# Kernel tuning notes

Hardware: AMD Instinct MI355X
Metric: run time of the kernel (lower is better)

Reference implementation:

```python
import jax, jax.numpy as jnp
import numpy as np

N_HEAD = 16
N_KV_HEAD = 4
HEAD_DIM = 128
EPS = 1e-6


def apply_rotary_emb(x, cos, sin):
    # x: (B,T,H,hd); cos/sin: (1,T,1,hd//2)
    d = x.shape[3] // 2
    x1, x2 = x[..., :d], x[..., d:]
    y1 = x1 * cos + x2 * sin
    y2 = x1 * -sin + x2 * cos
    return jnp.concatenate([y1, y2], axis=3).astype(x.dtype)


def rmsnorm(x):
    # flax nnx.RMSNorm with use_scale=False: x * rsqrt(mean(x^2) + eps)
    ms = jnp.mean(jnp.square(x), axis=-1, keepdims=True)
    return (x * jax.lax.rsqrt(ms + EPS)).astype(x.dtype)


def setup_inputs() -> dict:
    key = jax.random.key(0)
    ks = jax.random.split(key, 7)
    B, T, C = 4, 2048, 2048
    s = 0.02
    return {
        "x": jax.random.normal(ks[0], (B, T, C), jnp.float32),
        "cos": jax.random.normal(ks[1], (1, T, 1, HEAD_DIM // 2), jnp.float32),
        "sin": jax.random.normal(ks[2], (1, T, 1, HEAD_DIM // 2), jnp.float32),
        "Wq": jax.random.normal(ks[3], (C, N_HEAD * HEAD_DIM), jnp.float32) * s,
        "Wk": jax.random.normal(ks[4], (C, N_KV_HEAD * HEAD_DIM), jnp.float32) * s,
        "Wv": jax.random.normal(ks[5], (C, N_KV_HEAD * HEAD_DIM), jnp.float32) * s,
        "Wo": jax.random.normal(ks[6], (C, C), jnp.float32) * s,
    }


def reference(x, cos, sin, Wq, Wk, Wv, Wo):
    B, T, C = x.shape
    q = (x @ Wq).reshape(B, T, N_HEAD, HEAD_DIM)
    k = (x @ Wk).reshape(B, T, N_KV_HEAD, HEAD_DIM)
    v = (x @ Wv).reshape(B, T, N_KV_HEAD, HEAD_DIM)
    q = rmsnorm(apply_rotary_emb(q, cos, sin))
    k = rmsnorm(apply_rotary_emb(k, cos, sin))
    # (B,H,T,hd)
    q = jnp.transpose(q, (0, 2, 1, 3))
    k = jnp.transpose(k, (0, 2, 1, 3))
    v = jnp.transpose(v, (0, 2, 1, 3))
    nrep = N_HEAD // N_KV_HEAD
    k = jnp.repeat(k, nrep, axis=1)
    v = jnp.repeat(v, nrep, axis=1)
    scale = 1.0 / jnp.sqrt(jnp.float32(HEAD_DIM))
    att = jnp.einsum('bhqd,bhkd->bhqk', q, k) * scale
    mask = jnp.tril(jnp.ones((T, T), dtype=bool))[None, None, :, :]
    att = jnp.where(mask, att, -jnp.inf)
    att = jax.nn.softmax(att, axis=-1)
    y = jnp.einsum('bhqk,bhkd->bhqd', att, v)
    y = jnp.transpose(y, (0, 2, 1, 3)).reshape(B, T, -1)
    return y @ Wo
```

## Files before the change

### kernel.cpp

```cpp
#include <hip/hip_runtime.h>
#include <hip/hip_bf16.h>

typedef __attribute__((ext_vector_type(8))) short short8;
typedef __attribute__((ext_vector_type(4))) float f32x4;

#define B_SZ 4
#define T_SEQ 2048
#define C_DIM 2048
#define NH 16
#define NKV 4
#define HD 128

#define MFMA16 __builtin_amdgcn_mfma_f32_16x16x32_bf16

__device__ __forceinline__ unsigned short f2bf(float f) {
  union { __hip_bfloat16 h; unsigned short u; } v;
  v.h = __float2bfloat16(f);
  return v.u;
}
__device__ __forceinline__ float bf2f(unsigned short u) {
  union { unsigned short u; __hip_bfloat16 h; } v;
  v.u = u;
  return __bfloat162float(v.h);
}

__device__ __forceinline__ void gload_lds16(const unsigned short* g, unsigned short* l) {
  __builtin_amdgcn_global_load_lds(
      (const __attribute__((address_space(1))) unsigned int*)g,
      (__attribute__((address_space(3))) unsigned int*)l, 16, 0, 0);
}

__global__ void cast_x(const float* __restrict__ x, unsigned short* __restrict__ xb, int n4) {
  int i = blockIdx.x * blockDim.x + threadIdx.x;
  if (i < n4) {
    float4 f = ((const float4*)x)[i];
    ushort4 u = make_ushort4(f2bf(f.x), f2bf(f.y), f2bf(f.z), f2bf(f.w));
    ((ushort4*)xb)[i] = u;
  }
}

__global__ void wtrans(const float* __restrict__ W, unsigned short* __restrict__ Wt, int K, int N) {
  __shared__ float tile[32][33];
  int k0 = blockIdx.x * 32, n0 = blockIdx.y * 32;
  int tx = threadIdx.x, ty = threadIdx.y;
#pragma unroll
  for (int i = 0; i < 4; i++)
    tile[ty + i * 8][tx] = W[(size_t)(k0 + ty + i * 8) * N + n0 + tx];
  __syncthreads();
#pragma unroll
  for (int i = 0; i < 4; i++)
    Wt[(size_t)(n0 + ty + i * 8) * K + k0 + tx] = f2bf(tile[tx][ty + i * 8]);
}

__global__ void vtrans(const unsigned short* __restrict__ qkv, unsigned short* __restrict__ Vt) {
  __shared__ unsigned short tile[32][34];
  int t0 = blockIdx.x * 32, d0 = blockIdx.y * 32;
  int b = blockIdx.z >> 2, kvh = blockIdx.z & 3;
  int tx = threadIdx.x, ty = threadIdx.y;
#pragma unroll
  for (int i = 0; i < 4; i++)
    tile[ty + i * 8][tx] =
        qkv[(size_t)(b * T_SEQ + t0 + ty + i * 8) * 3072 + 2560 + kvh * HD + d0 + tx];
  __syncthreads();
#pragma unroll
  for (int i = 0; i < 4; i++)
    Vt[((size_t)(b * NKV + kvh) * HD + d0 + ty + i * 8) * T_SEQ + t0 + tx] = tile[tx][ty + i * 8];
}

template <typename OutT>
__global__ __launch_bounds__(512, 2) void gemm256(const unsigned short* __restrict__ A,
                                                  const unsigned short* __restrict__ Bt,
                                                  OutT* __restrict__ Cc, int N, int K, int GX) {
  __shared__ alignas(16) unsigned short lds[2][4][128 * 64];
  const int tid = threadIdx.x, lane = tid & 63, wid = tid >> 6;
  const int wave_m = wid >> 2, wave_n = wid & 3;
  const int r16 = lane & 15, q4 = lane >> 4;
  const int sw = r16 & 7;

  int nwg = gridDim.x, orig = blockIdx.x;
  int qq = nwg >> 3, rr = nwg & 7;
  int xcd = orig & 7, loc = orig >> 3;
  int wg = (xcd < rr ? xcd * (qq + 1) : rr * (qq + 1) + (xcd - rr) * qq) + loc;
  int bx = wg % GX, by = wg / GX;
  const size_t row0 = (size_t)bx * 256, col0 = (size_t)by * 256;

  const unsigned short* Ab0 = A + row0 * K;
  const unsigned short* Ab1 = A + (row0 + 128) * K;
  const unsigned short* Bb0 = Bt + col0 * K;
  const unsigned short* Bb1 = Bt + (col0 + 128) * K;

  const int srow = lane >> 3, spb = lane & 7;
  auto stage = [&](const unsigned short* base, int buf, int slot, int k0) {
#pragma unroll
    for (int j = 0; j < 2; ++j) {
      int cw = j * 8 + wid;
      int row = cw * 8 + srow;
      gload_lds16(base + (size_t)row * K + k0 + ((spb ^ srow) * 8), &lds[buf][slot][cw * 512]);
    }
  };

  f32x4 acc[8][4];
  f32x4 zero = {0.f, 0.f, 0.f, 0.f};
#pragma unroll
  for (int m = 0; m < 8; m++)
#pragma unroll
    for (int n = 0; n < 4; n++) acc[m][n] = zero;

  const int NT = K / 64;
  stage(Ab0, 0, 0, 0);
  stage(Ab1, 0, 1, 0);
  stage(Bb0, 0, 2, 0);
  stage(Bb1, 0, 3, 0);
  stage(Ab0, 1, 0, 64);
  stage(Ab1, 1, 1, 64);
  asm volatile("s_waitcnt vmcnt(4)" ::: "memory");
  __builtin_amdgcn_s_barrier();

  short8 af[4][2], b01[2][2], b23[2][2];
  const int bslot = 2 + (wave_n >> 1);
  const int bro = (wave_n & 1) * 64;

  int cur = 0;
#pragma unroll 1
  for (int t = 0; t < NT; ++t) {
    const unsigned short* Ah = &lds[cur][wave_m][0];
    const unsigned short* Bh = &lds[cur][bslot][0];
    const int k1 = t * 64 + 64, k2 = t * 64 + 128;
#pragma unroll
    for (int mf = 0; mf < 4; mf++)
#pragma unroll
      for (int kk = 0; kk < 2; kk++)
        af[mf][kk] = *(const short8*)(Ah + (mf * 16 + r16) * 64 + (((kk * 4 + q4) ^ sw) * 8));
#pragma unroll
    for (int nf = 0; nf < 2; nf++)
#pragma unroll
      for (int kk = 0; kk < 2; kk++)
        b01[nf][kk] =
            *(const short8*)(Bh + (bro + nf * 16 + r16) * 64 + (((kk * 4 + q4) ^ sw) * 8));
    if (t + 1 < NT) stage(Bb0, cur ^ 1, 2, k1);
    __builtin_amdgcn_s_barrier();
    asm volatile("s_waitcnt lgkmcnt(0)" ::: "memory");
    __builtin_amdgcn_s_setprio(1);
#pragma unroll
    for (int mf = 0; mf < 4; mf++)
#pragma unroll
      for (int nf = 0; nf < 2; nf++)
#pragma unroll
        for (int kk = 0; kk < 2; kk++)
          acc[mf][nf] = MFMA16(af[mf][kk], b01[nf][kk], acc[mf][nf], 0, 0, 0);
    __builtin_amdgcn_s_setprio(0);
    __builtin_amdgcn_s_barrier();
#pragma unroll
    for (int nf = 0; nf < 2; nf++)
#pragma unroll
      for (int kk = 0; kk < 2; kk++)
        b23[nf][kk] =
            *(const short8*)(Bh + (bro + (nf + 2) * 16 + r16) * 64 + (((kk * 4 + q4) ^ sw) * 8));
    if (t + 1 < NT) stage(Bb1, cur ^ 1, 3, k1);
    __builtin_amdgcn_s_barrier();
    asm volatile("s_waitcnt lgkmcnt(0)" ::: "memory");
    __builtin_amdgcn_s_setprio(1);
#pragma unroll
    for (int mf = 0; mf < 4; mf++)
#pragma unroll
      for (int nf = 0; nf < 2; nf++)
#pragma unroll
        for (int kk = 0; kk < 2; kk++)
          acc[mf][nf + 2] = MFMA16(af[mf][kk], b23[nf][kk], acc[mf][nf + 2], 0, 0, 0);
    __builtin_amdgcn_s_setprio(0);
    __builtin_amdgcn_s_barrier();
#pragma unroll
    for (int mf = 0; mf < 4; mf++)
#pragma unroll
      for (int kk = 0; kk < 2; kk++)
        af[mf][kk] =
            *(const short8*)(Ah + ((mf + 4) * 16 + r16) * 64 + (((kk * 4 + q4) ^ sw) * 8));
    __builtin_amdgcn_s_barrier();
    asm volatile("s_waitcnt lgkmcnt(0)" ::: "memory");
    __builtin_amdgcn_s_setprio(1);
#pragma unroll
    for (int mf = 0; mf < 4; mf++)
#pragma unroll
      for (int nf = 0; nf < 2; nf++)
#pragma unroll
        for (int kk = 0; kk < 2; kk++)
          acc[mf + 4][nf] = MFMA16(af[mf][kk], b01[nf][kk], acc[mf + 4][nf], 0, 0, 0);
    __builtin_amdgcn_s_setprio(0);
    __builtin_amdgcn_s_barrier();
    if (t + 2 < NT) {
      stage(Ab0, cur, 0, k2);
      stage(Ab1, cur, 1, k2);
    }
    __builtin_amdgcn_s_barrier();
    __builtin_amdgcn_s_setprio(1);
#pragma unroll
    for (int mf = 0; mf < 4; mf++)
#pragma unroll
      for (int nf = 0; nf < 2; nf++)
#pragma unroll
        for (int kk = 0; kk < 2; kk++)
          acc[mf + 4][nf + 2] = MFMA16(af[mf][kk], b23[nf][kk], acc[mf + 4][nf + 2], 0, 0, 0);
    __builtin_amdgcn_s_setprio(0);
    if (t + 1 < NT) {
      if (t + 2 < NT)
        asm volatile("s_waitcnt vmcnt(4)" ::: "memory");
      else
        asm volatile("s_waitcnt vmcnt(0)" ::: "memory");
    }
    __builtin_amdgcn_s_barrier();
    cur ^= 1;
  }

#pragma unroll
  for (int mf = 0; mf < 8; mf++)
#pragma unroll
    for (int nf = 0; nf < 4; nf++) {
      size_t rbase = row0 + wave_m * 128 + mf * 16 + q4 * 4;
      size_t cc = col0 + wave_n * 64 + nf * 16 + r16;
#pragma unroll
      for (int jj = 0; jj < 4; jj++) {
        if constexpr (sizeof(OutT) == 2)
          Cc[(rbase + jj) * (size_t)N + cc] = f2bf(acc[mf][nf][jj]);
        else
          Cc[(rbase + jj) * (size_t)N + cc] = acc[mf][nf][jj];
      }
    }
}

template <int NHEADS>
__global__ void ropenorm(const unsigned short* __restrict__ qkv, int colbase,
                         const float* __restrict__ cosp, const float* __restrict__ sinp,
                         unsigned short* __restrict__ qout, float outscale) {
  int gid = blockIdx.x * 4 + (threadIdx.x >> 6);
  int lane = threadIdx.x & 63;
  int h = gid % NHEADS;
  int bt = gid / NHEADS;
  int t = bt % T_SEQ, b = bt / T_SEQ;
  const unsigned short* src = qkv + (size_t)(b * T_SEQ + t) * 3072 + colbase + h * HD;
  float x1 = bf2f(src[lane]), x2 = bf2f(src[64 + lane]);
  float c = cosp[t * 64 + lane], s = sinp[t * 64 + lane];
  float y1 = x1 * c + x2 * s;
  float y2 = x2 * c - x1 * s;
  float ss = y1 * y1 + y2 * y2;
#pragma unroll
  for (int d = 1; d < 64; d <<= 1) ss += __shfl_xor(ss, d);
  float r = rsqrtf(ss * (1.f / 128.f) + 1e-6f) * outscale;
  unsigned short* dst = qout + ((size_t)(b * NHEADS + h) * T_SEQ + t) * HD;
  dst[lane] = f2bf(y1 * r);
  dst[64 + lane] = f2bf(y2 * r);
}

__device__ __forceinline__ int swzP(int row) {
  return (row & 7) ^ (((row >> 3) & 1) << 1);
}

__global__ __launch_bounds__(256, 2) void attn(const unsigned short* __restrict__ Qn,
                                               const unsigned short* __restrict__ Kn,
                                               const unsigned short* __restrict__ Vt,
                                               unsigned short* __restrict__ Y) {
  __shared__ alignas(16) unsigned short lK[2][64 * 128];
  __shared__ alignas(16) unsigned short lV[2][128 * 64];
  __shared__ alignas(16) unsigned short pl[4][32 * 64];

  int lin = blockIdx.x;
  int low3 = lin & 7, rest = lin >> 3;
  int chi = rest >> 6, idx = rest & 63;
  int c = (chi << 3) | low3;
  int b = c >> 2, kvh = c & 3;
  int h = kvh * 4 + (idx >> 4);
  int qt = 15 - (idx & 15);
  int Q0 = qt * 128;

  int lane = threadIdx.x & 63, w = threadIdx.x >> 6;
  const int r16 = lane & 15, q4 = lane >> 4;
  const unsigned short* Qp = Qn + ((size_t)(b * NH + h) * T_SEQ + Q0 + w * 32) * HD;
  const unsigned short* Kp = Kn + (size_t)(b * NKV + kvh) * T_SEQ * HD;
  const unsigned short* Vp = Vt + (size_t)(b * NKV + kvh) * HD * T_SEQ;

  short8 qf[2][4];
#pragma unroll
  for (int m = 0; m < 2; m++)
#pragma unroll
    for (int i = 0; i < 4; i++)
      qf[m][i] = *(const short8*)(Qp + (m * 16 + r16) * HD + i * 32 + q4 * 8);

  f32x4 zero = {0.f, 0.f, 0.f, 0.f};
  f32x4 o[2][8];
  float mrow[2][4], Lp[2][4];
#pragma unroll
  for (int m = 0; m < 2; m++) {
#pragma unroll
    for (int nb = 0; nb < 8; nb++) o[m][nb] = zero;
#pragma unroll
    for (int j = 0; j < 4; j++) { mrow[m][j] = -1e30f; Lp[m][j] = 0.f; }
  }

  auto stageK = [&](int kv0, int buf) {
#pragma unroll
    for (int j = 0; j < 4; ++j) {
      int cw = w * 4 + j;
      int row = cw * 4 + (lane >> 4);
      int cb = lane & 15;
      gload_lds16(Kp + (size_t)(kv0 + row) * HD + ((cb ^ (row & 7)) * 8), &lK[buf][cw * 512]);
    }
  };
  auto stageV = [&](int kv0, int buf) {
#pragma unroll
    for (int j = 0; j < 4; ++j) {
      int cw = w * 4 + j;
      int row = cw * 8 + (lane >> 3);
      int db = lane & 7;
      gload_lds16(Vp + (size_t)row * T_SEQ + kv0 + ((db ^ (row & 7)) * 8), &lV[buf][cw * 512]);
    }
  };

  const int ntiles = 2 * qt + 2;
  const int ntw = (Q0 + w * 32 + 95) >> 6;

  stageK(0, 0);
  stageV(0, 0);
  __syncthreads();
  int cur = 0;

  for (int t = 0; t < ntiles; ++t) {
    int kv0 = t * 64;
    if (t + 1 < ntiles) { stageK(kv0 + 64, cur ^ 1); stageV(kv0 + 64, cur ^ 1); }
    if (t < ntw) {
      f32x4 s[2][4];
      __builtin_amdgcn_s_setprio(1);
#pragma unroll
      for (int nt = 0; nt < 4; nt++) {
        f32x4 a0 = zero, a1 = zero;
        int krow = nt * 16 + r16;
#pragma unroll
        for (int i = 0; i < 4; i++) {
          short8 kf =
              *(const short8*)(&lK[cur][krow * 128 + ((q4 * 8 + i * 32) ^ ((krow & 7) << 3))]);
          a0 = __builtin_amdgcn_mfma_f32_16x16x32_bf16(qf[0][i], kf, a0, 0, 0, 0);
          a1 = __builtin_amdgcn_mfma_f32_16x16x32_bf16(qf[1][i], kf, a1, 0, 0, 0);
        }
        s[0][nt] = a0;
        s[1][nt] = a1;
      }
      __builtin_amdgcn_s_setprio(0);
      if (kv0 + 63 > Q0 + w * 32) {
#pragma unroll
        for (int m = 0; m < 2; m++)
#pragma unroll
          for (int nt = 0; nt < 4; nt++)
#pragma unroll
            for (int j = 0; j < 4; j++) {
              int col = kv0 + nt * 16 + r16;
              int row = Q0 + w * 32 + m * 16 + q4 * 4 + j;
              if (col > row) s[m][nt][j] = -1e30f;
            }
      }
      float pm[2][4];
#pragma unroll
      for (int m = 0; m < 2; m++)
#pragma unroll
        for (int j = 0; j < 4; j++)
          pm[m][j] = fmaxf(fmaxf(s[m][0][j], s[m][1][j]), fmaxf(s[m][2][j], s[m][3][j]));
#pragma unroll
      for (int d = 1; d < 16; d <<= 1)
#pragma unroll
        for (int m = 0; m < 2; m++)
#pragma unroll
          for (int j = 0; j < 4; j++) pm[m][j] = fmaxf(pm[m][j], __shfl_xor(pm[m][j], d));
      float dmax = -1e30f;
#pragma unroll
      for (int m = 0; m < 2; m++)
#pragma unroll
        for (int j = 0; j < 4; j++) dmax = fmaxf(dmax, pm[m][j] - mrow[m][j]);
      if (!__all(dmax <= 8.0f)) {
#pragma unroll
        for (int m = 0; m < 2; m++)
#pragma unroll
          for (int j = 0; j < 4; j++) {
            float mn = fmaxf(mrow[m][j], pm[m][j]);
            float al = __expf(mrow[m][j] - mn);
            mrow[m][j] = mn;
            Lp[m][j] *= al;
#pragma unroll
            for (int nb = 0; nb < 8; nb++) o[m][nb][j] *= al;
          }
      }
#pragma unroll
      for (int m = 0; m < 2; m++)
#pragma unroll
        for (int nt = 0; nt < 4; nt++)
#pragma unroll
          for (int j = 0; j < 4; j++) {
            float p = __expf(s[m][nt][j] - mrow[m][j]);
            Lp[m][j] += p;
            int prow = m * 16 + q4 * 4 + j;
            pl[w][prow * 64 + ((nt * 16 + r16) ^ (swzP(prow) << 3))] = f2bf(p);
          }
      __builtin_amdgcn_s_setprio(1);
#pragma unroll
      for (int ks = 0; ks < 2; ks++) {
        int t0 = ks * 32 + q4 * 8;
        int prow0 = r16, prow1 = 16 + r16;
        short8 pf0 = *(const short8*)(&pl[w][prow0 * 64 + (t0 ^ (swzP(prow0) << 3))]);
        short8 pf1 = *(const short8*)(&pl[w][prow1 * 64 + (t0 ^ (swzP(prow1) << 3))]);
#pragma unroll
        for (int nb = 0; nb < 8; nb++) {
          int vrow = nb * 16 + r16;
          short8 vf = *(const short8*)(&lV[cur][vrow * 64 + (t0 ^ ((vrow & 7) << 3))]);
          o[0][nb] = __builtin_amdgcn_mfma_f32_16x16x32_bf16(pf0, vf, o[0][nb], 0, 0, 0);
          o[1][nb] = __builtin_amdgcn_mfma_f32_16x16x32_bf16(pf1, vf, o[1][nb], 0, 0, 0);
        }
      }
      __builtin_amdgcn_s_setprio(0);
    }
    __syncthreads();
    cur ^= 1;
  }

  float linv[2][4];
#pragma unroll
  for (int m = 0; m < 2; m++)
#pragma unroll
    for (int j = 0; j < 4; j++) {
      float v = Lp[m][j];
#pragma unroll
      for (int d = 1; d < 16; d <<= 1) v += __shfl_xor(v, d);
      linv[m][j] = 1.f / v;
    }
#pragma unroll
  for (int m = 0; m < 2; m++)
#pragma unroll
    for (int nb = 0; nb < 8; nb++)
#pragma unroll
      for (int j = 0; j < 4; j++) {
        size_t row = (size_t)Q0 + w * 32 + m * 16 + q4 * 4 + j;
        Y[((size_t)(b * T_SEQ) + row) * (NH * HD) + h * HD + nb * 16 + r16] =
            f2bf(o[m][nb][j] * linv[m][j]);
      }
}

extern "C" void kernel_launch(void* const* d_in, const int* in_sizes, int n_in,
                              void* d_out, int out_size, void* d_ws, size_t ws_size,
                              hipStream_t stream) {
  const float* x = (const float*)d_in[0];
  const float* cosp = (const float*)d_in[1];
  const float* sinp = (const float*)d_in[2];
  const float* Wq = (const float*)d_in[3];
  const float* Wk = (const float*)d_in[4];
  const float* Wv = (const float*)d_in[5];
  const float* Wo = (const float*)d_in[6];
  float* out = (float*)d_out;

  char* ws = (char*)d_ws;
  size_t off = 0;
  auto alloc = [&](size_t bytes) { void* p = ws + off; off += bytes; return p; };
  const size_t BT = (size_t)B_SZ * T_SEQ;
  unsigned short* xb = (unsigned short*)alloc(BT * C_DIM * 2);
  unsigned short* WqkvT = (unsigned short*)alloc((size_t)3072 * 2048 * 2);
  unsigned short* WoT = (unsigned short*)alloc((size_t)2048 * 2048 * 2);
  unsigned short* qkv = (unsigned short*)alloc(BT * 3072 * 2);
  unsigned short* Kb = (unsigned short*)alloc(BT * 512 * 2);
  unsigned short* Vb = (unsigned short*)alloc(BT * 512 * 2);
  unsigned short* Qb = xb;
  unsigned short* Yb = qkv;

  dim3 tb(32, 8);
  cast_x<<<16384, 256, 0, stream>>>(x, xb, (int)(BT * C_DIM / 4));
  wtrans<<<dim3(64, 64), tb, 0, stream>>>(Wq, WqkvT, 2048, 2048);
  wtrans<<<dim3(64, 16), tb, 0, stream>>>(Wk, WqkvT + (size_t)2048 * 2048, 2048, 512);
  wtrans<<<dim3(64, 16), tb, 0, stream>>>(Wv, WqkvT + (size_t)2560 * 2048, 2048, 512);
  wtrans<<<dim3(64, 64), tb, 0, stream>>>(Wo, WoT, 2048, 2048);

  gemm256<unsigned short><<<384, 512, 0, stream>>>(xb, WqkvT, qkv, 3072, 2048, 32);

  ropenorm<NH><<<(B_SZ * T_SEQ * NH) / 4, 256, 0, stream>>>(qkv, 0, cosp, sinp, Qb,
                                                            0.08838834764831845f);
  ropenorm<NKV><<<(B_SZ * T_SEQ * NKV) / 4, 256, 0, stream>>>(qkv, 2048, cosp, sinp, Kb, 1.0f);
  vtrans<<<dim3(64, 4, 16), tb, 0, stream>>>(qkv, Vb);

  attn<<<dim3(1024), 256, 0, stream>>>(Qb, Kb, Vb, Yb);

  gemm256<float><<<256, 512, 0, stream>>>(Yb, WoT, out, 2048, 2048, 32);
}
```

Before: 434.6 us.

## Merge weight transposes and rope kernels; use 128x256 tiles for QKV GEMM

Folds the four weight-transpose launches into one kernel and the two rope/norm launches into one, which removes launch overhead and tail gaps between them. Replaces the 256x256-tile QKV projection GEMM with a new 128x256-tile kernel. That kernel splits B staging into two halves that are interleaved with MFMA phases, and it doubles the grid to 768 workgroups to fill the 256 CUs better. The cost is lower per-tile arithmetic intensity, so A and B are fetched more times per output.

```diff
diff --git a/kernel.cpp b/kernel.cpp
--- a/kernel.cpp
+++ b/kernel.cpp
@@ -39,9 +39,19 @@
   }
 }
 
-__global__ void wtrans(const float* __restrict__ W, unsigned short* __restrict__ Wt, int K, int N) {
+__global__ void wtransAll(const float* __restrict__ Wq, const float* __restrict__ Wk,
+                          const float* __restrict__ Wv, const float* __restrict__ Wo,
+                          unsigned short* __restrict__ WqkvT, unsigned short* __restrict__ WoT) {
   __shared__ float tile[32][33];
-  int k0 = blockIdx.x * 32, n0 = blockIdx.y * 32;
+  int y = blockIdx.y;
+  const float* W;
+  unsigned short* Wt;
+  int N, n0;
+  if (y < 64) { W = Wq; Wt = WqkvT; N = 2048; n0 = y * 32; }
+  else if (y < 80) { W = Wk; Wt = WqkvT + (size_t)2048 * 2048; N = 512; n0 = (y - 64) * 32; }
+  else if (y < 96) { W = Wv; Wt = WqkvT + (size_t)2560 * 2048; N = 512; n0 = (y - 80) * 32; }
+  else { W = Wo; Wt = WoT; N = 2048; n0 = (y - 96) * 32; }
+  int k0 = blockIdx.x * 32;
   int tx = threadIdx.x, ty = threadIdx.y;
 #pragma unroll
   for (int i = 0; i < 4; i++)
@@ -49,7 +59,7 @@
   __syncthreads();
 #pragma unroll
   for (int i = 0; i < 4; i++)
-    Wt[(size_t)(n0 + ty + i * 8) * K + k0 + tx] = f2bf(tile[tx][ty + i * 8]);
+    Wt[(size_t)(n0 + ty + i * 8) * 2048 + k0 + tx] = f2bf(tile[tx][ty + i * 8]);
 }
 
 __global__ void vtrans(const unsigned short* __restrict__ qkv, unsigned short* __restrict__ Vt) {
@@ -65,6 +75,130 @@
 #pragma unroll
   for (int i = 0; i < 4; i++)
     Vt[((size_t)(b * NKV + kvh) * HD + d0 + ty + i * 8) * T_SEQ + t0 + tx] = tile[tx][ty + i * 8];
+}
+
+template <typename OutT>
+__global__ __launch_bounds__(512, 2) void gemm128(const unsigned short* __restrict__ A,
+                                                  const unsigned short* __restrict__ Bt,
+                                                  OutT* __restrict__ Cc, int N, int K, int GX) {
+  __shared__ alignas(16) unsigned short lds[2][3][128 * 64];
+  const int tid = threadIdx.x, lane = tid & 63, wid = tid >> 6;
+  const int wave_m = wid >> 2, wave_n = wid & 3;
+  const int r16 = lane & 15, q4 = lane >> 4;
+  const int sw = r16 & 7;
+
+  int nwg = gridDim.x, orig = blockIdx.x;
+  int qq = nwg >> 3, rr = nwg & 7;
+  int xcd = orig & 7, loc = orig >> 3;
+  int wg = (xcd < rr ? xcd * (qq + 1) : rr * (qq + 1) + (xcd - rr) * qq) + loc;
+  int bx = wg % GX, by = wg / GX;
+  const size_t row0 = (size_t)bx * 128, col0 = (size_t)by * 256;
+
+  const unsigned short* Ab = A + row0 * K;
+  const unsigned short* Bb0 = Bt + col0 * K;
+  const unsigned short* Bb1 = Bt + (col0 + 128) * K;
+
+  const int srow = lane >> 3, spb = lane & 7;
+  auto stage = [&](const unsigned short* base, int buf, int slot, int k0) {
+#pragma unroll
+    for (int j = 0; j < 2; ++j) {
+      int cw = j * 8 + wid;
+      int row = cw * 8 + srow;
+      gload_lds16(base + (size_t)row * K + k0 + ((spb ^ srow) * 8), &lds[buf][slot][cw * 512]);
+    }
+  };
+
+  f32x4 acc[4][4];
+  f32x4 zero = {0.f, 0.f, 0.f, 0.f};
+#pragma unroll
+  for (int m = 0; m < 4; m++)
+#pragma unroll
+    for (int n = 0; n < 4; n++) acc[m][n] = zero;
+
+  const int NT = K / 64;
+  stage(Ab, 0, 0, 0);
+  stage(Bb0, 0, 1, 0);
+  stage(Bb1, 0, 2, 0);
+  stage(Ab, 1, 0, 64);
+  asm volatile("s_waitcnt vmcnt(2)" ::: "memory");
+  __builtin_amdgcn_s_barrier();
+
+  short8 af[4][2], b01[2][2], b23[2][2];
+  const int bslot = 1 + (wave_n >> 1);
+  const int bro = (wave_n & 1) * 64;
+
+  int cur = 0;
+#pragma unroll 1
+  for (int t = 0; t < NT; ++t) {
+    const unsigned short* Ah = &lds[cur][0][0];
+    const unsigned short* Bh = &lds[cur][bslot][0];
+    const int k1 = t * 64 + 64, k2 = t * 64 + 128;
+#pragma unroll
+    for (int mf = 0; mf < 4; mf++)
+#pragma unroll
+      for (int kk = 0; kk < 2; kk++)
+        af[mf][kk] =
+            *(const short8*)(Ah + (wave_m * 64 + mf * 16 + r16) * 64 + (((kk * 4 + q4) ^ sw) * 8));
+#pragma unroll
+    for (int nf = 0; nf < 2; nf++)
+#pragma unroll
+      for (int kk = 0; kk < 2; kk++)
+        b01[nf][kk] =
+            *(const short8*)(Bh + (bro + nf * 16 + r16) * 64 + (((kk * 4 + q4) ^ sw) * 8));
+    if (t + 1 < NT) stage(Bb0, cur ^ 1, 1, k1);
+    __builtin_amdgcn_s_barrier();
+    asm volatile("s_waitcnt lgkmcnt(0)" ::: "memory");
+    __builtin_amdgcn_s_setprio(1);
+#pragma unroll
+    for (int mf = 0; mf < 4; mf++)
+#pragma unroll
+      for (int nf = 0; nf < 2; nf++)
+#pragma unroll
+        for (int kk = 0; kk < 2; kk++)
+          acc[mf][nf] = MFMA16(af[mf][kk], b01[nf][kk], acc[mf][nf], 0, 0, 0);
+    __builtin_amdgcn_s_setprio(0);
+    __builtin_amdgcn_s_barrier();
+#pragma unroll
+    for (int nf = 0; nf < 2; nf++)
+#pragma unroll
+      for (int kk = 0; kk < 2; kk++)
+        b23[nf][kk] =
+            *(const short8*)(Bh + (bro + (nf + 2) * 16 + r16) * 64 + (((kk * 4 + q4) ^ sw) * 8));
+    if (t + 1 < NT) stage(Bb1, cur ^ 1, 2, k1);
+    if (t + 2 < NT) stage(Ab, cur, 0, k2);
+    __builtin_amdgcn_s_barrier();
+    asm volatile("s_waitcnt lgkmcnt(0)" ::: "memory");
+    __builtin_amdgcn_s_setprio(1);
+#pragma unroll
+    for (int mf = 0; mf < 4; mf++)
+#pragma unroll
+      for (int nf = 0; nf < 2; nf++)
+#pragma unroll
+        for (int kk = 0; kk < 2; kk++)
+          acc[mf][nf + 2] = MFMA16(af[mf][kk], b23[nf][kk], acc[mf][nf + 2], 0, 0, 0);
+    __builtin_amdgcn_s_setprio(0);
+    if (t + 2 < NT)
+      asm volatile("s_waitcnt vmcnt(2)" ::: "memory");
+    else if (t + 1 < NT)
+      asm volatile("s_waitcnt vmcnt(0)" ::: "memory");
+    __builtin_amdgcn_s_barrier();
+    cur ^= 1;
+  }
+
+#pragma unroll
+  for (int mf = 0; mf < 4; mf++)
+#pragma unroll
+    for (int nf = 0; nf < 4; nf++) {
+      size_t rbase = row0 + wave_m * 64 + mf * 16 + q4 * 4;
+      size_t cc = col0 + wave_n * 64 + nf * 16 + r16;
+#pragma unroll
+      for (int jj = 0; jj < 4; jj++) {
+        if constexpr (sizeof(OutT) == 2)
+          Cc[(rbase + jj) * (size_t)N + cc] = f2bf(acc[mf][nf][jj]);
+        else
+          Cc[(rbase + jj) * (size_t)N + cc] = acc[mf][nf][jj];
+      }
+    }
 }
 
 template <typename OutT>
@@ -227,16 +361,28 @@
     }
 }
 
-template <int NHEADS>
-__global__ void ropenorm(const unsigned short* __restrict__ qkv, int colbase,
-                         const float* __restrict__ cosp, const float* __restrict__ sinp,
-                         unsigned short* __restrict__ qout, float outscale) {
+__global__ void ropeAll(const unsigned short* __restrict__ qkv, const float* __restrict__ cosp,
+                        const float* __restrict__ sinp, unsigned short* __restrict__ Qb,
+                        unsigned short* __restrict__ Kb) {
   int gid = blockIdx.x * 4 + (threadIdx.x >> 6);
   int lane = threadIdx.x & 63;
-  int h = gid % NHEADS;
-  int bt = gid / NHEADS;
+  int hh = gid % 20;
+  int bt = gid / 20;
   int t = bt % T_SEQ, b = bt / T_SEQ;
-  const unsigned short* src = qkv + (size_t)(b * T_SEQ + t) * 3072 + colbase + h * HD;
+  int colbase;
+  unsigned short* dst;
+  float outscale;
+  if (hh < 16) {
+    colbase = hh * HD;
+    dst = Qb + ((size_t)(b * NH + hh) * T_SEQ + t) * HD;
+    outscale = 0.08838834764831845f;
+  } else {
+    int h2 = hh - 16;
+    colbase = 2048 + h2 * HD;
+    dst = Kb + ((size_t)(b * NKV + h2) * T_SEQ + t) * HD;
+    outscale = 1.0f;
+  }
+  const unsigned short* src = qkv + (size_t)(b * T_SEQ + t) * 3072 + colbase;
   float x1 = bf2f(src[lane]), x2 = bf2f(src[64 + lane]);
   float c = cosp[t * 64 + lane], s = sinp[t * 64 + lane];
   float y1 = x1 * c + x2 * s;
@@ -245,7 +391,6 @@
 #pragma unroll
   for (int d = 1; d < 64; d <<= 1) ss += __shfl_xor(ss, d);
   float r = rsqrtf(ss * (1.f / 128.f) + 1e-6f) * outscale;
-  unsigned short* dst = qout + ((size_t)(b * NHEADS + h) * T_SEQ + t) * HD;
   dst[lane] = f2bf(y1 * r);
   dst[64 + lane] = f2bf(y2 * r);
 }
@@ -466,16 +611,11 @@
 
   dim3 tb(32, 8);
   cast_x<<<16384, 256, 0, stream>>>(x, xb, (int)(BT * C_DIM / 4));
-  wtrans<<<dim3(64, 64), tb, 0, stream>>>(Wq, WqkvT, 2048, 2048);
-  wtrans<<<dim3(64, 16), tb, 0, stream>>>(Wk, WqkvT + (size_t)2048 * 2048, 2048, 512);
-  wtrans<<<dim3(64, 16), tb, 0, stream>>>(Wv, WqkvT + (size_t)2560 * 2048, 2048, 512);
-  wtrans<<<dim3(64, 64), tb, 0, stream>>>(Wo, WoT, 2048, 2048);
-
-  gemm256<unsigned short><<<384, 512, 0, stream>>>(xb, WqkvT, qkv, 3072, 2048, 32);
-
-  ropenorm<NH><<<(B_SZ * T_SEQ * NH) / 4, 256, 0, stream>>>(qkv, 0, cosp, sinp, Qb,
-                                                            0.08838834764831845f);
-  ropenorm<NKV><<<(B_SZ * T_SEQ * NKV) / 4, 256, 0, stream>>>(qkv, 2048, cosp, sinp, Kb, 1.0f);
+  wtransAll<<<dim3(64, 160), tb, 0, stream>>>(Wq, Wk, Wv, Wo, WqkvT, WoT);
+
+  gemm128<unsigned short><<<768, 512, 0, stream>>>(xb, WqkvT, qkv, 3072, 2048, 64);
+
+  ropeAll<<<(B_SZ * T_SEQ * 20) / 4, 256, 0, stream>>>(qkv, cosp, sinp, Qb, Kb);
   vtrans<<<dim3(64, 4, 16), tb, 0, stream>>>(qkv, Vb);
 
   attn<<<dim3(1024), 256, 0, stream>>>(Qb, Kb, Vb, Yb);
```

After: 426.3 us. No clear change (-1.9%).
